# Performance work log

Measured on AMD Instinct MI355X. Metric: run time of the kernel, lower is better.

Reference implementation:

```python
import jax, jax.numpy as jnp
import numpy as np

N = 50000


def gcn_conv(x, ei, W, b, n_nodes):
    """PyG GCNConv with default add_self_loops=True, symmetric normalization."""
    h = x @ W  # [N, hidden]
    loop = jnp.arange(n_nodes, dtype=ei.dtype)
    src = jnp.concatenate([ei[0], loop])
    dst = jnp.concatenate([ei[1], loop])
    # degree over destination nodes, unit edge weights (incl. self loops)
    deg = jax.ops.segment_sum(jnp.ones(src.shape[0], dtype=h.dtype), dst, num_segments=n_nodes)
    dinv = jnp.where(deg > 0, jax.lax.rsqrt(deg), 0.0)
    norm = dinv[src] * dinv[dst]  # [E+N]
    out = jax.ops.segment_sum(norm[:, None] * h[src], dst, num_segments=n_nodes)
    return out + b


def setup_inputs() -> dict:
    key = jax.random.key(0)
    ks = jax.random.split(key, 16)
    d_in, hidden, d_out, E = 64, 64, 3, 800000
    inp = {
        "x": jax.random.normal(ks[0], (N, d_in), dtype=jnp.float32),
        "ei_spring": jax.random.randint(ks[1], (2, E), 0, N, dtype=jnp.int32),
        "ei_damper": jax.random.randint(ks[2], (2, E), 0, N, dtype=jnp.int32),
        "W1s": jax.random.normal(ks[3], (d_in, hidden), dtype=jnp.float32) / np.sqrt(d_in),
        "b1s": jnp.zeros((hidden,), dtype=jnp.float32),
        "W1d": jax.random.normal(ks[4], (d_in, hidden), dtype=jnp.float32) / np.sqrt(d_in),
        "b1d": jnp.zeros((hidden,), dtype=jnp.float32),
        "W2s": jax.random.normal(ks[5], (hidden, hidden), dtype=jnp.float32) / np.sqrt(hidden),
        "b2s": jnp.zeros((hidden,), dtype=jnp.float32),
        "W2d": jax.random.normal(ks[6], (hidden, hidden), dtype=jnp.float32) / np.sqrt(hidden),
        "b2d": jnp.zeros((hidden,), dtype=jnp.float32),
        "Wlin": jax.random.normal(ks[7], (hidden, d_out), dtype=jnp.float32) / np.sqrt(hidden),
        "blin": jnp.zeros((d_out,), dtype=jnp.float32),
    }
    return inp


def reference(x, ei_spring, ei_damper, W1s, b1s, W1d, b1d, W2s, b2s, W2d, b2d, Wlin, blin):
    # layer 1: HeteroConv sum over both relations, then ReLU
    h = gcn_conv(x, ei_spring, W1s, b1s, N) + gcn_conv(x, ei_damper, W1d, b1d, N)
    h = jax.nn.relu(h)
    # layer 2
    h = gcn_conv(h, ei_spring, W2s, b2s, N) + gcn_conv(h, ei_damper, W2d, b2d, N)
    h = jax.nn.relu(h)
    return h @ Wlin + blin
```

## Files before the change

### kernel.cpp

```cpp
#include <hip/hip_runtime.h>
#include <hip/hip_fp16.h>

#define NN 50000
#define BSHIFT 8
#define NBK ((NN + 255) >> 8)
#define CHUNK 4096
#define CAP 8192

typedef __attribute__((ext_vector_type(8))) _Float16 f16x8;
typedef __attribute__((ext_vector_type(4))) float f32x4;

__device__ __forceinline__ float recw(unsigned r) {
    unsigned short us = (unsigned short)(r >> 16);
    __half h;
    __builtin_memcpy(&h, &us, 2);
    return __half2float(h);
}
__device__ __forceinline__ float2 h2f2(unsigned v) {
    __half2 h;
    __builtin_memcpy(&h, &v, 4);
    return __half22float2(h);
}
__device__ __forceinline__ unsigned f2h2(float a, float b) {
    __half2 h = __floats2half2_rn(a, b);
    unsigned u;
    __builtin_memcpy(&u, &h, 4);
    return u;
}
__device__ __forceinline__ f16x8 as_f16x8(uint4 v) {
    f16x8 r;
    __builtin_memcpy(&r, &v, 16);
    return r;
}
__device__ __forceinline__ unsigned short f2h1(float v) {
    __half h = __float2half(v);
    unsigned short us;
    __builtin_memcpy(&us, &h, 2);
    return us;
}


__global__ __launch_bounds__(256) void cvt_x(const float* __restrict__ x,
                                             unsigned* __restrict__ x16, int total4) {
    int i = blockIdx.x * 256 + threadIdx.x;
    if (i >= total4) return;
    float4 v = reinterpret_cast<const float4*>(x)[i];
    uint2 o;
    o.x = f2h2(v.x, v.y);
    o.y = f2h2(v.z, v.w);
    reinterpret_cast<uint2*>(x16)[i] = o;
}


__global__ __launch_bounds__(256) void prep_w(const float* __restrict__ W1s,
                                              const float* __restrict__ W1d,
                                              const float* __restrict__ W2s,
                                              const float* __restrict__ W2d,
                                              unsigned short* __restrict__ Bp) {
    int idx = blockIdx.x * 256 + threadIdx.x;
    if (idx >= 16384) return;
    int layer = idx >> 13;
    int rem = idx & 8191;
    int j = rem & 7;
    int l = (rem >> 3) & 63;
    int jt = (rem >> 9) & 3;
    int ks = rem >> 11;
    int k = ks * 32 + (l >> 4) * 8 + j;
    int col = jt * 16 + (l & 15);
    const float* Ws = layer ? W2s : W1s;
    const float* Wd = layer ? W2d : W1d;
    float v = (k < 64) ? Ws[k * 64 + col] : Wd[(k - 64) * 64 + col];
    Bp[idx] = f2h1(v);
}


__global__ __launch_bounds__(256) void bucket_count(const int* __restrict__ eiS, int Es,
                                                    const int* __restrict__ eiD, int Ed,
                                                    int* __restrict__ cntS,
                                                    int* __restrict__ cntD) {
    __shared__ int h[NBK];
    int rel = blockIdx.y;
    const int* dst = rel ? (eiD + Ed) : (eiS + Es);
    int E = rel ? Ed : Es;
    int* cnt = rel ? cntD : cntS;
    int base = blockIdx.x * CHUNK;
    if (base >= E) return;
    for (int i = threadIdx.x; i < NBK; i += 256) h[i] = 0;
    __syncthreads();
    int end = (base + CHUNK < E) ? base + CHUNK : E;
    for (int e = base + threadIdx.x; e < end; e += 256)
        atomicAdd(&h[dst[e] >> BSHIFT], 1);
    __syncthreads();
    for (int i = threadIdx.x; i < NBK; i += 256)
        if (h[i]) atomicAdd(&cnt[i], h[i]);
}


__global__ __launch_bounds__(256) void bucket_scan(const int* __restrict__ cntS,
                                                   const int* __restrict__ cntD,
                                                   int* __restrict__ baseS,
                                                   int* __restrict__ baseD,
                                                   int* __restrict__ curS,
                                                   int* __restrict__ curD,
                                                   int* __restrict__ offsS,
                                                   int* __restrict__ offsD) {
    __shared__ int sA[256], sB[256];
    const int* cnt = blockIdx.x ? cntD : cntS;
    int* base = blockIdx.x ? baseD : baseS;
    int* cur  = blockIdx.x ? curD : curS;
    int* offs = blockIdx.x ? offsD : offsS;
    int t = threadIdx.x;
    int v = (t < NBK) ? cnt[t] : 0;
    sA[t] = v;
    __syncthreads();
    int* pin = sA; int* pout = sB;
    for (int st = 1; st < 256; st <<= 1) {
        int x = pin[t];
        if (t >= st) x += pin[t - st];
        pout[t] = x;
        __syncthreads();
        int* tmp = pin; pin = pout; pout = tmp;
    }
    int incl = pin[t];
    int excl = incl - v;
    if (t < NBK) { base[t] = excl; cur[t] = excl; }
    if (t == NBK - 1) { base[NBK] = incl; offs[NN] = incl; }
}


__global__ __launch_bounds__(256) void bucket_scatter(const int* __restrict__ eiS, int Es,
                                                      const int* __restrict__ eiD, int Ed,
                                                      int* __restrict__ curS,
                                                      int* __restrict__ curD,
                                                      unsigned* __restrict__ recS,
                                                      unsigned* __restrict__ recD) {
    __shared__ int h[NBK];
    __shared__ int rb[NBK];
    int rel = blockIdx.y;
    const int* ei = rel ? eiD : eiS;
    int E = rel ? Ed : Es;
    int* cur = rel ? curD : curS;
    unsigned* rec = rel ? recD : recS;
    int base = blockIdx.x * CHUNK;
    if (base >= E) return;
    const int* src = ei;
    const int* dst = ei + E;
    int end = (base + CHUNK < E) ? base + CHUNK : E;

    for (int i = threadIdx.x; i < NBK; i += 256) h[i] = 0;
    __syncthreads();
    for (int e = base + threadIdx.x; e < end; e += 256)
        atomicAdd(&h[dst[e] >> BSHIFT], 1);
    __syncthreads();
    for (int i = threadIdx.x; i < NBK; i += 256) {
        int c = h[i];
        rb[i] = c ? atomicAdd(&cur[i], c) : 0;
    }
    __syncthreads();
    for (int i = threadIdx.x; i < NBK; i += 256) h[i] = 0;
    __syncthreads();
    for (int e = base + threadIdx.x; e < end; e += 256) {
        int d = dst[e];
        int s = src[e];
        int b = d >> BSHIFT;
        int p = atomicAdd(&h[b], 1);
        rec[rb[b] + p] = (unsigned)s | ((unsigned)(d & 255) << 16);
    }
}


__global__ __launch_bounds__(256) void bucket_finalize(const int* __restrict__ baseS,
                                                       const int* __restrict__ baseD,
                                                       unsigned* __restrict__ recS,
                                                       unsigned* __restrict__ recD,
                                                       int* __restrict__ offsS,
                                                       int* __restrict__ offsD,
                                                       float* __restrict__ dinvS,
                                                       float* __restrict__ dinvD) {
    __shared__ unsigned recs[CAP];
    __shared__ int lc[256], sA[256], sB[256];
    int rel = blockIdx.y;
    const int* base = rel ? baseD : baseS;
    unsigned* rec = rel ? recD : recS;
    int* offs = rel ? offsD : offsS;
    float* dinv = rel ? dinvD : dinvS;
    int b = blockIdx.x;
    int b0 = base[b], b1 = base[b + 1];
    int cnt = b1 - b0;
    int t = threadIdx.x;
    lc[t] = 0;
    __syncthreads();
    for (int i = t; i < cnt; i += 256) {
        unsigned r = rec[b0 + i];
        if (i < CAP) recs[i] = r;
        atomicAdd(&lc[r >> 16], 1);
    }
    __syncthreads();
    int v = lc[t];
    int g = (b << BSHIFT) + t;
    if (g < NN) dinv[g] = rsqrtf((float)v + 1.0f);
    sA[t] = v;
    __syncthreads();
    int* pin = sA; int* pout = sB;
    for (int st = 1; st < 256; st <<= 1) {
        int x = pin[t];
        if (t >= st) x += pin[t - st];
        pout[t] = x;
        __syncthreads();
        int* tmp = pin; pin = pout; pout = tmp;
    }
    int excl = pin[t] - v;
    if (g < NN) offs[g] = b0 + excl;
    lc[t] = excl;
    __syncthreads();
    for (int i = t; i < cnt; i += 256) {
        unsigned r = (i < CAP) ? recs[i] : rec[b0 + i];
        int p = atomicAdd(&lc[r >> 16], 1);
        rec[b0 + p] = r & 0xFFFFu;
    }
}


__global__ __launch_bounds__(256) void pack_rec(unsigned* __restrict__ recS, int Es,
                                                unsigned* __restrict__ recD, int Ed,
                                                const float* __restrict__ dinvS,
                                                const float* __restrict__ dinvD) {
    int i = blockIdx.x * 256 + threadIdx.x;
    if (i < Es) {
        unsigned s = recS[i] & 0xFFFFu;
        recS[i] = s | ((unsigned)f2h1(dinvS[s]) << 16);
    }
    if (i < Ed) {
        unsigned s = recD[i] & 0xFFFFu;
        recD[i] = s | ((unsigned)f2h1(dinvD[s]) << 16);
    }
}


__global__ __launch_bounds__(256) void gather_agg(const int* __restrict__ offsS,
                                                  const unsigned* __restrict__ recS,
                                                  const int* __restrict__ offsD,
                                                  const unsigned* __restrict__ recD,
                                                  const unsigned* __restrict__ feat,
                                                  const float* __restrict__ dinvS,
                                                  const float* __restrict__ dinvD,
                                                  unsigned* __restrict__ A, int n) {
    int wid = (blockIdx.x * 256 + threadIdx.x) >> 6;
    int lane = threadIdx.x & 63;
    if (wid >= n) return;
    int g = lane >> 4;
    int q = lane & 15;

    const uint2* featv = reinterpret_cast<const uint2*>(feat);

    float dS = dinvS[wid];
    float dD = dinvD[wid];

    int eS0 = offsS[wid], eS1 = offsS[wid + 1];
    int eD0 = offsD[wid], eD1 = offsD[wid + 1];
    int nbS = (eS1 - eS0 + 3) >> 2;
    int nbD = (eD1 - eD0 + 3) >> 2;

    uint2 sv = featv[(size_t)wid * 16 + q];
    float2 s0 = h2f2(sv.x), s1 = h2f2(sv.y);
    float wself = (g == 0) ? dS : 0.0f;
    float wselfD = (g == 0) ? dD : 0.0f;
    float aS0 = wself * s0.x, aS1 = wself * s0.y, aS2 = wself * s1.x, aS3 = wself * s1.y;
    float aD0 = wselfD * s0.x, aD1 = wselfD * s0.y, aD2 = wselfD * s1.x, aD3 = wselfD * s1.y;

#define BODY_S(I)                                                              \
    {                                                                          \
        int e = eS0 + 4 * (I) + g;                                             \
        unsigned r = (e < eS1) ? recS[e] : 0u;                                 \
        uint2 v = featv[(size_t)(r & 0xFFFFu) * 16 + q];                       \
        float w = recw(r);                                                     \
        float2 f0 = h2f2(v.x), f1 = h2f2(v.y);                                 \
        aS0 = fmaf(w, f0.x, aS0); aS1 = fmaf(w, f0.y, aS1);                    \
        aS2 = fmaf(w, f1.x, aS2); aS3 = fmaf(w, f1.y, aS3);                    \
    }
#define BODY_D(I)                                                              \
    {                                                                          \
        int e = eD0 + 4 * (I) + g;                                             \
        unsigned r = (e < eD1) ? recD[e] : 0u;                                 \
        uint2 v = featv[(size_t)(r & 0xFFFFu) * 16 + q];                       \
        float w = recw(r);                                                     \
        float2 f0 = h2f2(v.x), f1 = h2f2(v.y);                                 \
        aD0 = fmaf(w, f0.x, aD0); aD1 = fmaf(w, f0.y, aD1);                    \
        aD2 = fmaf(w, f1.x, aD2); aD3 = fmaf(w, f1.y, aD3);                    \
    }

    int nb = (nbS < nbD) ? nbS : nbD;
    int i = 0;
#pragma unroll 2
    for (; i < nb; i++) {
        BODY_S(i)
        BODY_D(i)
    }
#pragma unroll 2
    for (int is = i; is < nbS; is++) BODY_S(is)
#pragma unroll 2
    for (int id = i; id < nbD; id++) BODY_D(id)

#undef BODY_S
#undef BODY_D

#pragma unroll
    for (int st = 16; st <= 32; st <<= 1) {
        aS0 += __shfl_xor(aS0, st, 64);
        aS1 += __shfl_xor(aS1, st, 64);
        aS2 += __shfl_xor(aS2, st, 64);
        aS3 += __shfl_xor(aS3, st, 64);
        aD0 += __shfl_xor(aD0, st, 64);
        aD1 += __shfl_xor(aD1, st, 64);
        aD2 += __shfl_xor(aD2, st, 64);
        aD3 += __shfl_xor(aD3, st, 64);
    }

    if (g == 0) {
        uint2 oS, oD;
        oS.x = f2h2(dS * aS0, dS * aS1);
        oS.y = f2h2(dS * aS2, dS * aS3);
        oD.x = f2h2(dD * aD0, dD * aD1);
        oD.y = f2h2(dD * aD2, dD * aD3);
        reinterpret_cast<uint2*>(A + (size_t)wid * 64)[q] = oS;
        reinterpret_cast<uint2*>(A + (size_t)wid * 64 + 32)[q] = oD;
    }
}


#define STORE_JT(ACC, JT)                                                     \
    {                                                                         \
        int colj = (JT) * 16 + lr;                                            \
        float bs = ba[colj] + bb[colj];                                       \
        _Pragma("unroll")                                                     \
        for (int r = 0; r < 4; r++) {                                         \
            float v = fmaxf(ACC[r] + bs, 0.0f);                               \
            outH[(size_t)(m0 + lh * 4 + r) * 64 + colj] = f2h1(v);            \
        }                                                                     \
    }

#define HEAD_JT(ACC, JT)                                                      \
    {                                                                         \
        int colj = (JT) * 16 + lr;                                            \
        float bs = ba[colj] + bb[colj];                                       \
        float w0 = Wlin[colj * 3 + 0];                                        \
        float w1 = Wlin[colj * 3 + 1];                                        \
        float w2 = Wlin[colj * 3 + 2];                                        \
        _Pragma("unroll")                                                     \
        for (int r = 0; r < 4; r++) {                                         \
            float v = fmaxf(ACC[r] + bs, 0.0f);                               \
            h0[r] = fmaf(v, w0, h0[r]);                                       \
            h1[r] = fmaf(v, w1, h1[r]);                                       \
            h2[r] = fmaf(v, w2, h2[r]);                                       \
        }                                                                     \
    }

template <int HEAD>
__global__ __launch_bounds__(256) void apply_mfma(const unsigned* __restrict__ A,
                                                  const unsigned short* __restrict__ Bp,
                                                  const float* __restrict__ ba,
                                                  const float* __restrict__ bb,
                                                  const float* __restrict__ Wlin,
                                                  const float* __restrict__ blin,
                                                  unsigned short* __restrict__ outH,
                                                  float* __restrict__ out3, int n) {
    int wid = (blockIdx.x * 256 + threadIdx.x) >> 6;
    int l = threadIdx.x & 63;
    int m0 = wid * 16;
    if (m0 >= n) return;
    int lr = l & 15;
    int lh = l >> 4;

    const uint4* Bv = reinterpret_cast<const uint4*>(Bp);
    f32x4 acc0 = {0.f, 0.f, 0.f, 0.f};
    f32x4 acc1 = {0.f, 0.f, 0.f, 0.f};
    f32x4 acc2 = {0.f, 0.f, 0.f, 0.f};
    f32x4 acc3 = {0.f, 0.f, 0.f, 0.f};

#pragma unroll
    for (int ks = 0; ks < 4; ks++) {
        uint4 av = *reinterpret_cast<const uint4*>(A + (size_t)(m0 + lr) * 64 + ks * 16 + lh * 4);
        f16x8 af = as_f16x8(av);
        uint4 b0 = Bv[(ks * 4 + 0) * 64 + l];
        uint4 b1 = Bv[(ks * 4 + 1) * 64 + l];
        uint4 b2 = Bv[(ks * 4 + 2) * 64 + l];
        uint4 b3 = Bv[(ks * 4 + 3) * 64 + l];
        acc0 = __builtin_amdgcn_mfma_f32_16x16x32_f16(af, as_f16x8(b0), acc0, 0, 0, 0);
        acc1 = __builtin_amdgcn_mfma_f32_16x16x32_f16(af, as_f16x8(b1), acc1, 0, 0, 0);
        acc2 = __builtin_amdgcn_mfma_f32_16x16x32_f16(af, as_f16x8(b2), acc2, 0, 0, 0);
        acc3 = __builtin_amdgcn_mfma_f32_16x16x32_f16(af, as_f16x8(b3), acc3, 0, 0, 0);
    }

    if (HEAD == 0) {
        STORE_JT(acc0, 0)
        STORE_JT(acc1, 1)
        STORE_JT(acc2, 2)
        STORE_JT(acc3, 3)
    } else {
        float h0[4] = {0.f, 0.f, 0.f, 0.f};
        float h1[4] = {0.f, 0.f, 0.f, 0.f};
        float h2[4] = {0.f, 0.f, 0.f, 0.f};
        HEAD_JT(acc0, 0)
        HEAD_JT(acc1, 1)
        HEAD_JT(acc2, 2)
        HEAD_JT(acc3, 3)
#pragma unroll
        for (int st = 1; st < 16; st <<= 1) {
#pragma unroll
            for (int r = 0; r < 4; r++) {
                h0[r] += __shfl_xor(h0[r], st, 64);
                h1[r] += __shfl_xor(h1[r], st, 64);
                h2[r] += __shfl_xor(h2[r], st, 64);
            }
        }
        if (lr == 0) {
#pragma unroll
            for (int r = 0; r < 4; r++) {
                int row = m0 + lh * 4 + r;
                out3[row * 3 + 0] = h0[r] + blin[0];
                out3[row * 3 + 1] = h1[r] + blin[1];
                out3[row * 3 + 2] = h2[r] + blin[2];
            }
        }
    }
}

extern "C" void kernel_launch(void* const* d_in, const int* in_sizes, int n_in,
                              void* d_out, int out_size, void* d_ws, size_t ws_size,
                              hipStream_t stream) {
    const float* x    = (const float*)d_in[0];
    const int*   eis  = (const int*)d_in[1];
    const int*   eid  = (const int*)d_in[2];
    const float* W1s  = (const float*)d_in[3];
    const float* b1s  = (const float*)d_in[4];
    const float* W1d  = (const float*)d_in[5];
    const float* b1d  = (const float*)d_in[6];
    const float* W2s  = (const float*)d_in[7];
    const float* b2s  = (const float*)d_in[8];
    const float* W2d  = (const float*)d_in[9];
    const float* b2d  = (const float*)d_in[10];
    const float* Wlin = (const float*)d_in[11];
    const float* blin = (const float*)d_in[12];

    const int N  = NN;
    const int Es = in_sizes[1] / 2;
    const int Ed = in_sizes[2] / 2;
    int Emax = (Es > Ed) ? Es : Ed;

    int*   cntS  = (int*)d_ws;
    int*   cntD  = cntS + NBK;
    int*   baseS = cntD + NBK;
    int*   baseD = baseS + (NBK + 4);
    int*   curS  = baseD + (NBK + 4);
    int*   curD  = curS + NBK;
    int*   offsS = curD + NBK;
    int*   offsD = offsS + (N + 4);
    float* dinvS = (float*)(offsD + (N + 4));
    float* dinvD = dinvS + N;
    unsigned* recS = (unsigned*)(dinvD + N);
    unsigned* recD = recS + Es;
    unsigned* x16  = recD + Ed;
    unsigned* h16u = x16 + (size_t)N * 32;
    unsigned* Abuf = h16u + (size_t)N * 32;
    unsigned short* Bp = (unsigned short*)(Abuf + (size_t)N * 64);
    unsigned short* h16 = (unsigned short*)h16u;

    hipMemsetAsync(cntS, 0, (size_t)2 * NBK * sizeof(int), stream);
    cvt_x<<<(N * 16 + 255) / 256, 256, 0, stream>>>(x, x16, N * 16);
    prep_w<<<64, 256, 0, stream>>>(W1s, W1d, W2s, W2d, Bp);
    dim3 egrid((Emax + CHUNK - 1) / CHUNK, 2);
    bucket_count<<<egrid, 256, 0, stream>>>(eis, Es, eid, Ed, cntS, cntD);
    bucket_scan<<<2, 256, 0, stream>>>(cntS, cntD, baseS, baseD, curS, curD, offsS, offsD);
    bucket_scatter<<<egrid, 256, 0, stream>>>(eis, Es, eid, Ed, curS, curD, recS, recD);
    dim3 fgrid(NBK, 2);
    bucket_finalize<<<fgrid, 256, 0, stream>>>(baseS, baseD, recS, recD, offsS, offsD,
                                               dinvS, dinvD);
    pack_rec<<<(Emax + 255) / 256, 256, 0, stream>>>(recS, Es, recD, Ed, dinvS, dinvD);

    int gatherBlocks = (N * 64 + 255) / 256;
    int mtiles = (N + 15) / 16;
    int applyBlocks = (mtiles * 64 + 255) / 256;

    gather_agg<<<gatherBlocks, 256, 0, stream>>>(offsS, recS, offsD, recD, x16,
                                                 dinvS, dinvD, Abuf, N);
    apply_mfma<0><<<applyBlocks, 256, 0, stream>>>(Abuf, Bp, b1s, b1d,
                                                   nullptr, nullptr, h16, nullptr, N);

    gather_agg<<<gatherBlocks, 256, 0, stream>>>(offsS, recS, offsD, recD, h16u,
                                                 dinvS, dinvD, Abuf, N);
    apply_mfma<1><<<applyBlocks, 256, 0, stream>>>(Abuf, Bp + 8192, b2s, b2d,
                                                   Wlin, blin, nullptr, (float*)d_out, N);
}
```

Measured before the change: 176.9 us.

## Merge prep kernels and remap gather to one node per quarter-wave per relation

Fuses x conversion, weight packing and bucket counting into one launch with a 3-row grid, removing two kernel launches. Gather now assigns each 16-lane group its own node and relation, using a 2D grid over relations, so there is no cross-group shuffle reduction. Each group loops over its own edge list in steps of four, with a wave-wide any() to handle divergent degrees. This removes the shuffles and spreads work over more waves, at the cost of divergence across the four nodes in a wave and a larger prep grid where many blocks exit early.

```diff
diff --git a/kernel.cpp b/kernel.cpp
--- a/kernel.cpp
+++ b/kernel.cpp
@@ -40,59 +40,58 @@
 }
 
 
-__global__ __launch_bounds__(256) void cvt_x(const float* __restrict__ x,
-                                             unsigned* __restrict__ x16, int total4) {
-    int i = blockIdx.x * 256 + threadIdx.x;
-    if (i >= total4) return;
-    float4 v = reinterpret_cast<const float4*>(x)[i];
-    uint2 o;
-    o.x = f2h2(v.x, v.y);
-    o.y = f2h2(v.z, v.w);
-    reinterpret_cast<uint2*>(x16)[i] = o;
-}
-
-
-__global__ __launch_bounds__(256) void prep_w(const float* __restrict__ W1s,
-                                              const float* __restrict__ W1d,
-                                              const float* __restrict__ W2s,
-                                              const float* __restrict__ W2d,
-                                              unsigned short* __restrict__ Bp) {
-    int idx = blockIdx.x * 256 + threadIdx.x;
-    if (idx >= 16384) return;
-    int layer = idx >> 13;
-    int rem = idx & 8191;
-    int j = rem & 7;
-    int l = (rem >> 3) & 63;
-    int jt = (rem >> 9) & 3;
-    int ks = rem >> 11;
-    int k = ks * 32 + (l >> 4) * 8 + j;
-    int col = jt * 16 + (l & 15);
-    const float* Ws = layer ? W2s : W1s;
-    const float* Wd = layer ? W2d : W1d;
-    float v = (k < 64) ? Ws[k * 64 + col] : Wd[(k - 64) * 64 + col];
-    Bp[idx] = f2h1(v);
-}
-
-
-__global__ __launch_bounds__(256) void bucket_count(const int* __restrict__ eiS, int Es,
-                                                    const int* __restrict__ eiD, int Ed,
-                                                    int* __restrict__ cntS,
-                                                    int* __restrict__ cntD) {
+__global__ __launch_bounds__(256) void fat_prep(const int* __restrict__ eiS, int Es,
+                                                const int* __restrict__ eiD, int Ed,
+                                                int* __restrict__ cntS,
+                                                int* __restrict__ cntD,
+                                                const float* __restrict__ x,
+                                                unsigned* __restrict__ x16, int total4,
+                                                const float* __restrict__ W1s,
+                                                const float* __restrict__ W1d,
+                                                const float* __restrict__ W2s,
+                                                const float* __restrict__ W2d,
+                                                unsigned short* __restrict__ Bp) {
     __shared__ int h[NBK];
-    int rel = blockIdx.y;
-    const int* dst = rel ? (eiD + Ed) : (eiS + Es);
-    int E = rel ? Ed : Es;
-    int* cnt = rel ? cntD : cntS;
-    int base = blockIdx.x * CHUNK;
-    if (base >= E) return;
-    for (int i = threadIdx.x; i < NBK; i += 256) h[i] = 0;
-    __syncthreads();
-    int end = (base + CHUNK < E) ? base + CHUNK : E;
-    for (int e = base + threadIdx.x; e < end; e += 256)
-        atomicAdd(&h[dst[e] >> BSHIFT], 1);
-    __syncthreads();
-    for (int i = threadIdx.x; i < NBK; i += 256)
-        if (h[i]) atomicAdd(&cnt[i], h[i]);
+    if (blockIdx.y < 2) {
+        int rel = blockIdx.y;
+        const int* dst = rel ? (eiD + Ed) : (eiS + Es);
+        int E = rel ? Ed : Es;
+        int* cnt = rel ? cntD : cntS;
+        int base = blockIdx.x * CHUNK;
+        if (base >= E) return;
+        for (int i = threadIdx.x; i < NBK; i += 256) h[i] = 0;
+        __syncthreads();
+        int end = (base + CHUNK < E) ? base + CHUNK : E;
+        for (int e = base + threadIdx.x; e < end; e += 256)
+            atomicAdd(&h[dst[e] >> BSHIFT], 1);
+        __syncthreads();
+        for (int i = threadIdx.x; i < NBK; i += 256)
+            if (h[i]) atomicAdd(&cnt[i], h[i]);
+    } else {
+        int i = blockIdx.x * 256 + threadIdx.x;
+        if (i < total4) {
+            float4 v = reinterpret_cast<const float4*>(x)[i];
+            uint2 o;
+            o.x = f2h2(v.x, v.y);
+            o.y = f2h2(v.z, v.w);
+            reinterpret_cast<uint2*>(x16)[i] = o;
+        }
+        if (blockIdx.x < 64) {
+            int idx = blockIdx.x * 256 + threadIdx.x;
+            int layer = idx >> 13;
+            int rem = idx & 8191;
+            int j = rem & 7;
+            int l = (rem >> 3) & 63;
+            int jt = (rem >> 9) & 3;
+            int ks = rem >> 11;
+            int k = ks * 32 + (l >> 4) * 8 + j;
+            int col = jt * 16 + (l & 15);
+            const float* Ws = layer ? W2s : W1s;
+            const float* Wd = layer ? W2d : W1d;
+            float v = (k < 64) ? Ws[k * 64 + col] : Wd[(k - 64) * 64 + col];
+            Bp[idx] = f2h1(v);
+        }
+    }
 }
 
 
@@ -245,86 +244,49 @@
                                                   const float* __restrict__ dinvS,
                                                   const float* __restrict__ dinvD,
                                                   unsigned* __restrict__ A, int n) {
-    int wid = (blockIdx.x * 256 + threadIdx.x) >> 6;
+    int rel = blockIdx.y;
+    const int* __restrict__ offs = rel ? offsD : offsS;
+    const unsigned* __restrict__ rec = rel ? recD : recS;
+    const float* __restrict__ dinv = rel ? dinvD : dinvS;
+
+    int wv = (blockIdx.x * 256 + threadIdx.x) >> 6;
     int lane = threadIdx.x & 63;
-    if (wid >= n) return;
-    int g = lane >> 4;
+    int c = lane >> 4;
     int q = lane & 15;
+    int node = wv * 4 + c;
+    if (node >= n) return;
 
     const uint2* featv = reinterpret_cast<const uint2*>(feat);
 
-    float dS = dinvS[wid];
-    float dD = dinvD[wid];
-
-    int eS0 = offsS[wid], eS1 = offsS[wid + 1];
-    int eD0 = offsD[wid], eD1 = offsD[wid + 1];
-    int nbS = (eS1 - eS0 + 3) >> 2;
-    int nbD = (eD1 - eD0 + 3) >> 2;
-
-    uint2 sv = featv[(size_t)wid * 16 + q];
+    float dv = dinv[node];
+    int e0 = offs[node];
+    int cnt = offs[node + 1] - e0;
+
+    uint2 sv = featv[(size_t)node * 16 + q];
     float2 s0 = h2f2(sv.x), s1 = h2f2(sv.y);
-    float wself = (g == 0) ? dS : 0.0f;
-    float wselfD = (g == 0) ? dD : 0.0f;
-    float aS0 = wself * s0.x, aS1 = wself * s0.y, aS2 = wself * s1.x, aS3 = wself * s1.y;
-    float aD0 = wselfD * s0.x, aD1 = wselfD * s0.y, aD2 = wselfD * s1.x, aD3 = wselfD * s1.y;
-
-#define BODY_S(I)                                                              \
-    {                                                                          \
-        int e = eS0 + 4 * (I) + g;                                             \
-        unsigned r = (e < eS1) ? recS[e] : 0u;                                 \
-        uint2 v = featv[(size_t)(r & 0xFFFFu) * 16 + q];                       \
-        float w = recw(r);                                                     \
-        float2 f0 = h2f2(v.x), f1 = h2f2(v.y);                                 \
-        aS0 = fmaf(w, f0.x, aS0); aS1 = fmaf(w, f0.y, aS1);                    \
-        aS2 = fmaf(w, f1.x, aS2); aS3 = fmaf(w, f1.y, aS3);                    \
-    }
-#define BODY_D(I)                                                              \
-    {                                                                          \
-        int e = eD0 + 4 * (I) + g;                                             \
-        unsigned r = (e < eD1) ? recD[e] : 0u;                                 \
-        uint2 v = featv[(size_t)(r & 0xFFFFu) * 16 + q];                       \
-        float w = recw(r);                                                     \
-        float2 f0 = h2f2(v.x), f1 = h2f2(v.y);                                 \
-        aD0 = fmaf(w, f0.x, aD0); aD1 = fmaf(w, f0.y, aD1);                    \
-        aD2 = fmaf(w, f1.x, aD2); aD3 = fmaf(w, f1.y, aD3);                    \
-    }
-
-    int nb = (nbS < nbD) ? nbS : nbD;
+    float a0 = dv * s0.x, a1 = dv * s0.y, a2 = dv * s1.x, a3 = dv * s1.y;
+
     int i = 0;
-#pragma unroll 2
-    for (; i < nb; i++) {
-        BODY_S(i)
-        BODY_D(i)
-    }
-#pragma unroll 2
-    for (int is = i; is < nbS; is++) BODY_S(is)
-#pragma unroll 2
-    for (int id = i; id < nbD; id++) BODY_D(id)
-
-#undef BODY_S
-#undef BODY_D
-
+    while (__any(i < cnt)) {
 #pragma unroll
-    for (int st = 16; st <= 32; st <<= 1) {
-        aS0 += __shfl_xor(aS0, st, 64);
-        aS1 += __shfl_xor(aS1, st, 64);
-        aS2 += __shfl_xor(aS2, st, 64);
-        aS3 += __shfl_xor(aS3, st, 64);
-        aD0 += __shfl_xor(aD0, st, 64);
-        aD1 += __shfl_xor(aD1, st, 64);
-        aD2 += __shfl_xor(aD2, st, 64);
-        aD3 += __shfl_xor(aD3, st, 64);
-    }
-
-    if (g == 0) {
-        uint2 oS, oD;
-        oS.x = f2h2(dS * aS0, dS * aS1);
-        oS.y = f2h2(dS * aS2, dS * aS3);
-        oD.x = f2h2(dD * aD0, dD * aD1);
-        oD.y = f2h2(dD * aD2, dD * aD3);
-        reinterpret_cast<uint2*>(A + (size_t)wid * 64)[q] = oS;
-        reinterpret_cast<uint2*>(A + (size_t)wid * 64 + 32)[q] = oD;
-    }
+        for (int k = 0; k < 4; k++) {
+            int e = i + k;
+            unsigned r = (e < cnt) ? rec[e0 + e] : 0u;
+            uint2 v = featv[(size_t)(r & 0xFFFFu) * 16 + q];
+            float wt = recw(r);
+            float2 f0 = h2f2(v.x), f1 = h2f2(v.y);
+            a0 = fmaf(wt, f0.x, a0);
+            a1 = fmaf(wt, f0.y, a1);
+            a2 = fmaf(wt, f1.x, a2);
+            a3 = fmaf(wt, f1.y, a3);
+        }
+        i += 4;
+    }
+
+    uint2 o;
+    o.x = f2h2(dv * a0, dv * a1);
+    o.y = f2h2(dv * a2, dv * a3);
+    reinterpret_cast<uint2*>(A)[(size_t)node * 32 + rel * 16 + q] = o;
 }
 
 
@@ -466,28 +428,28 @@
     unsigned short* h16 = (unsigned short*)h16u;
 
     hipMemsetAsync(cntS, 0, (size_t)2 * NBK * sizeof(int), stream);
-    cvt_x<<<(N * 16 + 255) / 256, 256, 0, stream>>>(x, x16, N * 16);
-    prep_w<<<64, 256, 0, stream>>>(W1s, W1d, W2s, W2d, Bp);
+    dim3 pgrid(3125, 3);
+    fat_prep<<<pgrid, 256, 0, stream>>>(eis, Es, eid, Ed, cntS, cntD,
+                                        x, x16, N * 16, W1s, W1d, W2s, W2d, Bp);
+    bucket_scan<<<2, 256, 0, stream>>>(cntS, cntD, baseS, baseD, curS, curD, offsS, offsD);
     dim3 egrid((Emax + CHUNK - 1) / CHUNK, 2);
-    bucket_count<<<egrid, 256, 0, stream>>>(eis, Es, eid, Ed, cntS, cntD);
-    bucket_scan<<<2, 256, 0, stream>>>(cntS, cntD, baseS, baseD, curS, curD, offsS, offsD);
     bucket_scatter<<<egrid, 256, 0, stream>>>(eis, Es, eid, Ed, curS, curD, recS, recD);
     dim3 fgrid(NBK, 2);
     bucket_finalize<<<fgrid, 256, 0, stream>>>(baseS, baseD, recS, recD, offsS, offsD,
                                                dinvS, dinvD);
     pack_rec<<<(Emax + 255) / 256, 256, 0, stream>>>(recS, Es, recD, Ed, dinvS, dinvD);
 
-    int gatherBlocks = (N * 64 + 255) / 256;
+    dim3 ggrid((N + 15) / 16, 2);
     int mtiles = (N + 15) / 16;
     int applyBlocks = (mtiles * 64 + 255) / 256;
 
-    gather_agg<<<gatherBlocks, 256, 0, stream>>>(offsS, recS, offsD, recD, x16,
-                                                 dinvS, dinvD, Abuf, N);
+    gather_agg<<<ggrid, 256, 0, stream>>>(offsS, recS, offsD, recD, x16,
+                                          dinvS, dinvD, Abuf, N);
     apply_mfma<0><<<applyBlocks, 256, 0, stream>>>(Abuf, Bp, b1s, b1d,
                                                    nullptr, nullptr, h16, nullptr, N);
 
-    gather_agg<<<gatherBlocks, 256, 0, stream>>>(offsS, recS, offsD, recD, h16u,
-                                                 dinvS, dinvD, Abuf, N);
+    gather_agg<<<ggrid, 256, 0, stream>>>(offsS, recS, offsD, recD, h16u,
+                                          dinvS, dinvD, Abuf, N);
     apply_mfma<1><<<applyBlocks, 256, 0, stream>>>(Abuf, Bp + 8192, b2s, b2d,
                                                    Wlin, blin, nullptr, (float*)d_out, N);
 }
```

Result: no change. 178.6 us (+1.0%).

## Fuse prep kernels, compute degrees early, fold dinv packing into finalize

Applied to the files above, without the earlier changes.

Merges x conversion, weight packing and bucket counting into one launch, and adds global atomic degree counting there so dinv can be computed in the scan kernel. The finalize kernel then writes the fp16 dinv of each source directly into the sorted records, which removes the separate pack_rec pass over all edges. This cuts three launches and one full read-write pass of the edge records. In exchange it adds global atomics on degree counters and a larger memset. Many grid blocks in the count part exit immediately, since the grid is sized for the x conversion.

```diff
diff --git a/kernel.cpp b/kernel.cpp
--- a/kernel.cpp
+++ b/kernel.cpp
@@ -40,59 +40,64 @@
 }
 
 
-__global__ __launch_bounds__(256) void cvt_x(const float* __restrict__ x,
-                                             unsigned* __restrict__ x16, int total4) {
-    int i = blockIdx.x * 256 + threadIdx.x;
-    if (i >= total4) return;
-    float4 v = reinterpret_cast<const float4*>(x)[i];
-    uint2 o;
-    o.x = f2h2(v.x, v.y);
-    o.y = f2h2(v.z, v.w);
-    reinterpret_cast<uint2*>(x16)[i] = o;
-}
-
-
-__global__ __launch_bounds__(256) void prep_w(const float* __restrict__ W1s,
-                                              const float* __restrict__ W1d,
-                                              const float* __restrict__ W2s,
-                                              const float* __restrict__ W2d,
-                                              unsigned short* __restrict__ Bp) {
-    int idx = blockIdx.x * 256 + threadIdx.x;
-    if (idx >= 16384) return;
-    int layer = idx >> 13;
-    int rem = idx & 8191;
-    int j = rem & 7;
-    int l = (rem >> 3) & 63;
-    int jt = (rem >> 9) & 3;
-    int ks = rem >> 11;
-    int k = ks * 32 + (l >> 4) * 8 + j;
-    int col = jt * 16 + (l & 15);
-    const float* Ws = layer ? W2s : W1s;
-    const float* Wd = layer ? W2d : W1d;
-    float v = (k < 64) ? Ws[k * 64 + col] : Wd[(k - 64) * 64 + col];
-    Bp[idx] = f2h1(v);
-}
-
-
-__global__ __launch_bounds__(256) void bucket_count(const int* __restrict__ eiS, int Es,
-                                                    const int* __restrict__ eiD, int Ed,
-                                                    int* __restrict__ cntS,
-                                                    int* __restrict__ cntD) {
+__global__ __launch_bounds__(256) void fat_prep(const int* __restrict__ eiS, int Es,
+                                                const int* __restrict__ eiD, int Ed,
+                                                int* __restrict__ cntS,
+                                                int* __restrict__ cntD,
+                                                int* __restrict__ degS,
+                                                int* __restrict__ degD,
+                                                const float* __restrict__ x,
+                                                unsigned* __restrict__ x16, int total4,
+                                                const float* __restrict__ W1s,
+                                                const float* __restrict__ W1d,
+                                                const float* __restrict__ W2s,
+                                                const float* __restrict__ W2d,
+                                                unsigned short* __restrict__ Bp) {
     __shared__ int h[NBK];
-    int rel = blockIdx.y;
-    const int* dst = rel ? (eiD + Ed) : (eiS + Es);
-    int E = rel ? Ed : Es;
-    int* cnt = rel ? cntD : cntS;
-    int base = blockIdx.x * CHUNK;
-    if (base >= E) return;
-    for (int i = threadIdx.x; i < NBK; i += 256) h[i] = 0;
-    __syncthreads();
-    int end = (base + CHUNK < E) ? base + CHUNK : E;
-    for (int e = base + threadIdx.x; e < end; e += 256)
-        atomicAdd(&h[dst[e] >> BSHIFT], 1);
-    __syncthreads();
-    for (int i = threadIdx.x; i < NBK; i += 256)
-        if (h[i]) atomicAdd(&cnt[i], h[i]);
+    if (blockIdx.y < 2) {
+        int rel = blockIdx.y;
+        const int* dst = rel ? (eiD + Ed) : (eiS + Es);
+        int E = rel ? Ed : Es;
+        int* cnt = rel ? cntD : cntS;
+        int* deg = rel ? degD : degS;
+        int base = blockIdx.x * CHUNK;
+        if (base >= E) return;
+        for (int i = threadIdx.x; i < NBK; i += 256) h[i] = 0;
+        __syncthreads();
+        int end = (base + CHUNK < E) ? base + CHUNK : E;
+        for (int e = base + threadIdx.x; e < end; e += 256) {
+            int d = dst[e];
+            atomicAdd(&h[d >> BSHIFT], 1);
+            atomicAdd(&deg[d], 1);
+        }
+        __syncthreads();
+        for (int i = threadIdx.x; i < NBK; i += 256)
+            if (h[i]) atomicAdd(&cnt[i], h[i]);
+    } else {
+        int i = blockIdx.x * 256 + threadIdx.x;
+        if (i < total4) {
+            float4 v = reinterpret_cast<const float4*>(x)[i];
+            uint2 o;
+            o.x = f2h2(v.x, v.y);
+            o.y = f2h2(v.z, v.w);
+            reinterpret_cast<uint2*>(x16)[i] = o;
+        }
+        if (blockIdx.x < 64) {
+            int idx = blockIdx.x * 256 + threadIdx.x;
+            int layer = idx >> 13;
+            int rem = idx & 8191;
+            int j = rem & 7;
+            int l = (rem >> 3) & 63;
+            int jt = (rem >> 9) & 3;
+            int ks = rem >> 11;
+            int k = ks * 32 + (l >> 4) * 8 + j;
+            int col = jt * 16 + (l & 15);
+            const float* Ws = layer ? W2s : W1s;
+            const float* Wd = layer ? W2d : W1d;
+            float v = (k < 64) ? Ws[k * 64 + col] : Wd[(k - 64) * 64 + col];
+            Bp[idx] = f2h1(v);
+        }
+    }
 }
 
 
@@ -103,13 +108,26 @@
                                                    int* __restrict__ curS,
                                                    int* __restrict__ curD,
                                                    int* __restrict__ offsS,
-                                                   int* __restrict__ offsD) {
+                                                   int* __restrict__ offsD,
+                                                   const int* __restrict__ degS,
+                                                   const int* __restrict__ degD,
+                                                   float* __restrict__ dinvS,
+                                                   float* __restrict__ dinvD) {
+    int t = threadIdx.x;
+    if (blockIdx.x >= 2) {
+        int g = (blockIdx.x - 2) * 256 + t;
+        if (g < NN) {
+            dinvS[g] = rsqrtf((float)degS[g] + 1.0f);
+            dinvD[g] = rsqrtf((float)degD[g] + 1.0f);
+        }
+        return;
+    }
     __shared__ int sA[256], sB[256];
-    const int* cnt = blockIdx.x ? cntD : cntS;
-    int* base = blockIdx.x ? baseD : baseS;
-    int* cur  = blockIdx.x ? curD : curS;
-    int* offs = blockIdx.x ? offsD : offsS;
-    int t = threadIdx.x;
+    int r = blockIdx.x;
+    const int* cnt = r ? cntD : cntS;
+    int* base = r ? baseD : baseS;
+    int* cur  = r ? curD : curS;
+    int* offs = r ? offsD : offsS;
     int v = (t < NBK) ? cnt[t] : 0;
     sA[t] = v;
     __syncthreads();
@@ -175,15 +193,15 @@
                                                        unsigned* __restrict__ recD,
                                                        int* __restrict__ offsS,
                                                        int* __restrict__ offsD,
-                                                       float* __restrict__ dinvS,
-                                                       float* __restrict__ dinvD) {
+                                                       const float* __restrict__ dinvS,
+                                                       const float* __restrict__ dinvD) {
     __shared__ unsigned recs[CAP];
     __shared__ int lc[256], sA[256], sB[256];
     int rel = blockIdx.y;
     const int* base = rel ? baseD : baseS;
     unsigned* rec = rel ? recD : recS;
     int* offs = rel ? offsD : offsS;
-    float* dinv = rel ? dinvD : dinvS;
+    const float* dinv = rel ? dinvD : dinvS;
     int b = blockIdx.x;
     int b0 = base[b], b1 = base[b + 1];
     int cnt = b1 - b0;
@@ -198,7 +216,6 @@
     __syncthreads();
     int v = lc[t];
     int g = (b << BSHIFT) + t;
-    if (g < NN) dinv[g] = rsqrtf((float)v + 1.0f);
     sA[t] = v;
     __syncthreads();
     int* pin = sA; int* pout = sB;
@@ -216,23 +233,8 @@
     for (int i = t; i < cnt; i += 256) {
         unsigned r = (i < CAP) ? recs[i] : rec[b0 + i];
         int p = atomicAdd(&lc[r >> 16], 1);
-        rec[b0 + p] = r & 0xFFFFu;
-    }
-}
-
-
-__global__ __launch_bounds__(256) void pack_rec(unsigned* __restrict__ recS, int Es,
-                                                unsigned* __restrict__ recD, int Ed,
-                                                const float* __restrict__ dinvS,
-                                                const float* __restrict__ dinvD) {
-    int i = blockIdx.x * 256 + threadIdx.x;
-    if (i < Es) {
-        unsigned s = recS[i] & 0xFFFFu;
-        recS[i] = s | ((unsigned)f2h1(dinvS[s]) << 16);
-    }
-    if (i < Ed) {
-        unsigned s = recD[i] & 0xFFFFu;
-        recD[i] = s | ((unsigned)f2h1(dinvD[s]) << 16);
+        unsigned s = r & 0xFFFFu;
+        rec[b0 + p] = s | ((unsigned)f2h1(dinv[s]) << 16);
     }
 }
 
@@ -449,7 +451,9 @@
 
     int*   cntS  = (int*)d_ws;
     int*   cntD  = cntS + NBK;
-    int*   baseS = cntD + NBK;
+    int*   degS  = cntD + NBK;
+    int*   degD  = degS + N;
+    int*   baseS = degD + N;
     int*   baseD = baseS + (NBK + 4);
     int*   curS  = baseD + (NBK + 4);
     int*   curD  = curS + NBK;
@@ -465,17 +469,17 @@
     unsigned short* Bp = (unsigned short*)(Abuf + (size_t)N * 64);
     unsigned short* h16 = (unsigned short*)h16u;
 
-    hipMemsetAsync(cntS, 0, (size_t)2 * NBK * sizeof(int), stream);
-    cvt_x<<<(N * 16 + 255) / 256, 256, 0, stream>>>(x, x16, N * 16);
-    prep_w<<<64, 256, 0, stream>>>(W1s, W1d, W2s, W2d, Bp);
+    hipMemsetAsync(cntS, 0, ((size_t)2 * NBK + (size_t)2 * N) * sizeof(int), stream);
+    dim3 pgrid(3125, 3);
+    fat_prep<<<pgrid, 256, 0, stream>>>(eis, Es, eid, Ed, cntS, cntD, degS, degD,
+                                        x, x16, N * 16, W1s, W1d, W2s, W2d, Bp);
+    bucket_scan<<<2 + NBK, 256, 0, stream>>>(cntS, cntD, baseS, baseD, curS, curD,
+                                             offsS, offsD, degS, degD, dinvS, dinvD);
     dim3 egrid((Emax + CHUNK - 1) / CHUNK, 2);
-    bucket_count<<<egrid, 256, 0, stream>>>(eis, Es, eid, Ed, cntS, cntD);
-    bucket_scan<<<2, 256, 0, stream>>>(cntS, cntD, baseS, baseD, curS, curD, offsS, offsD);
     bucket_scatter<<<egrid, 256, 0, stream>>>(eis, Es, eid, Ed, curS, curD, recS, recD);
     dim3 fgrid(NBK, 2);
     bucket_finalize<<<fgrid, 256, 0, stream>>>(baseS, baseD, recS, recD, offsS, offsD,
                                                dinvS, dinvD);
-    pack_rec<<<(Emax + 255) / 256, 256, 0, stream>>>(recS, Es, recD, Ed, dinvS, dinvD);
 
     int gatherBlocks = (N * 64 + 255) / 256;
     int mtiles = (N + 15) / 16;
```

Result: slower. 222.3 us (+25.7%).

## Sub-bucket edges by source range and fuse prep kernels into one launch

Applied to the files above, without the earlier changes.

The edge bucketing now classifies each edge by destination bucket and also by source range (8 sub-classes), so records within a destination bucket are grouped by source. The aim is better locality on the source-feature gathers in the aggregation. The count, x conversion and weight packing kernels are merged into one multi-role launch to cut launch overhead. The scan now runs serially over about 1600 classes in chunks, and the shared histograms are 8x larger, which adds LDS pressure and atomic work. The finalize kernel may re-sort within each bucket, which would undo part of the source grouping.

```diff
diff --git a/kernel.cpp b/kernel.cpp
--- a/kernel.cpp
+++ b/kernel.cpp
@@ -4,6 +4,9 @@
 #define NN 50000
 #define BSHIFT 8
 #define NBK ((NN + 255) >> 8)
+#define NR 8
+#define RSH 13
+#define NCLS (NBK * NR)
 #define CHUNK 4096
 #define CAP 8192
 
@@ -40,91 +43,111 @@
 }
 
 
-__global__ __launch_bounds__(256) void cvt_x(const float* __restrict__ x,
-                                             unsigned* __restrict__ x16, int total4) {
-    int i = blockIdx.x * 256 + threadIdx.x;
-    if (i >= total4) return;
-    float4 v = reinterpret_cast<const float4*>(x)[i];
-    uint2 o;
-    o.x = f2h2(v.x, v.y);
-    o.y = f2h2(v.z, v.w);
-    reinterpret_cast<uint2*>(x16)[i] = o;
-}
-
-
-__global__ __launch_bounds__(256) void prep_w(const float* __restrict__ W1s,
-                                              const float* __restrict__ W1d,
-                                              const float* __restrict__ W2s,
-                                              const float* __restrict__ W2d,
-                                              unsigned short* __restrict__ Bp) {
-    int idx = blockIdx.x * 256 + threadIdx.x;
-    if (idx >= 16384) return;
-    int layer = idx >> 13;
-    int rem = idx & 8191;
-    int j = rem & 7;
-    int l = (rem >> 3) & 63;
-    int jt = (rem >> 9) & 3;
-    int ks = rem >> 11;
-    int k = ks * 32 + (l >> 4) * 8 + j;
-    int col = jt * 16 + (l & 15);
-    const float* Ws = layer ? W2s : W1s;
-    const float* Wd = layer ? W2d : W1d;
-    float v = (k < 64) ? Ws[k * 64 + col] : Wd[(k - 64) * 64 + col];
-    Bp[idx] = f2h1(v);
-}
-
-
-__global__ __launch_bounds__(256) void bucket_count(const int* __restrict__ eiS, int Es,
-                                                    const int* __restrict__ eiD, int Ed,
-                                                    int* __restrict__ cntS,
-                                                    int* __restrict__ cntD) {
-    __shared__ int h[NBK];
-    int rel = blockIdx.y;
-    const int* dst = rel ? (eiD + Ed) : (eiS + Es);
-    int E = rel ? Ed : Es;
-    int* cnt = rel ? cntD : cntS;
-    int base = blockIdx.x * CHUNK;
-    if (base >= E) return;
-    for (int i = threadIdx.x; i < NBK; i += 256) h[i] = 0;
-    __syncthreads();
-    int end = (base + CHUNK < E) ? base + CHUNK : E;
-    for (int e = base + threadIdx.x; e < end; e += 256)
-        atomicAdd(&h[dst[e] >> BSHIFT], 1);
-    __syncthreads();
-    for (int i = threadIdx.x; i < NBK; i += 256)
-        if (h[i]) atomicAdd(&cnt[i], h[i]);
-}
-
-
-__global__ __launch_bounds__(256) void bucket_scan(const int* __restrict__ cntS,
-                                                   const int* __restrict__ cntD,
-                                                   int* __restrict__ baseS,
-                                                   int* __restrict__ baseD,
-                                                   int* __restrict__ curS,
-                                                   int* __restrict__ curD,
-                                                   int* __restrict__ offsS,
-                                                   int* __restrict__ offsD) {
-    __shared__ int sA[256], sB[256];
+__global__ __launch_bounds__(256) void fat_prep(const int* __restrict__ eiS, int Es,
+                                                const int* __restrict__ eiD, int Ed,
+                                                int* __restrict__ cntS,
+                                                int* __restrict__ cntD,
+                                                const float* __restrict__ x,
+                                                unsigned* __restrict__ x16, int total4,
+                                                const float* __restrict__ W1s,
+                                                const float* __restrict__ W1d,
+                                                const float* __restrict__ W2s,
+                                                const float* __restrict__ W2d,
+                                                unsigned short* __restrict__ Bp) {
+    __shared__ int h[NCLS];
+    if (blockIdx.y < 2) {
+        int rel = blockIdx.y;
+        const int* ei = rel ? eiD : eiS;
+        int E = rel ? Ed : Es;
+        int* cnt = rel ? cntD : cntS;
+        int base = blockIdx.x * CHUNK;
+        if (base >= E) return;
+        const int* src = ei;
+        const int* dst = ei + E;
+        for (int i = threadIdx.x; i < NCLS; i += 256) h[i] = 0;
+        __syncthreads();
+        int end = (base + CHUNK < E) ? base + CHUNK : E;
+        for (int e = base + threadIdx.x; e < end; e += 256) {
+            int cls = (dst[e] >> BSHIFT) * NR + (src[e] >> RSH);
+            atomicAdd(&h[cls], 1);
+        }
+        __syncthreads();
+        for (int i = threadIdx.x; i < NCLS; i += 256)
+            if (h[i]) atomicAdd(&cnt[i], h[i]);
+    } else {
+        int i = blockIdx.x * 256 + threadIdx.x;
+        if (i < total4) {
+            float4 v = reinterpret_cast<const float4*>(x)[i];
+            uint2 o;
+            o.x = f2h2(v.x, v.y);
+            o.y = f2h2(v.z, v.w);
+            reinterpret_cast<uint2*>(x16)[i] = o;
+        }
+        if (blockIdx.x < 64) {
+            int idx = blockIdx.x * 256 + threadIdx.x;
+            int layer = idx >> 13;
+            int rem = idx & 8191;
+            int j = rem & 7;
+            int l = (rem >> 3) & 63;
+            int jt = (rem >> 9) & 3;
+            int ks = rem >> 11;
+            int k = ks * 32 + (l >> 4) * 8 + j;
+            int col = jt * 16 + (l & 15);
+            const float* Ws = layer ? W2s : W1s;
+            const float* Wd = layer ? W2d : W1d;
+            float v = (k < 64) ? Ws[k * 64 + col] : Wd[(k - 64) * 64 + col];
+            Bp[idx] = f2h1(v);
+        }
+    }
+}
+
+
+__global__ __launch_bounds__(256) void cls_scan(const int* __restrict__ cntS,
+                                                const int* __restrict__ cntD,
+                                                int* __restrict__ baseS,
+                                                int* __restrict__ baseD,
+                                                int* __restrict__ curS,
+                                                int* __restrict__ curD,
+                                                int* __restrict__ offsS,
+                                                int* __restrict__ offsD) {
     const int* cnt = blockIdx.x ? cntD : cntS;
     int* base = blockIdx.x ? baseD : baseS;
     int* cur  = blockIdx.x ? curD : curS;
     int* offs = blockIdx.x ? offsD : offsS;
+    __shared__ int sA[256], sB[256];
+    __shared__ int carry_s;
     int t = threadIdx.x;
-    int v = (t < NBK) ? cnt[t] : 0;
-    sA[t] = v;
-    __syncthreads();
-    int* pin = sA; int* pout = sB;
-    for (int st = 1; st < 256; st <<= 1) {
-        int x = pin[t];
-        if (t >= st) x += pin[t - st];
-        pout[t] = x;
+    if (t == 0) carry_s = 0;
+    __syncthreads();
+    int nchunk = (NCLS + 255) / 256;
+    for (int c = 0; c < nchunk; ++c) {
+        int i = c * 256 + t;
+        int v = (i < NCLS) ? cnt[i] : 0;
+        sA[t] = v;
         __syncthreads();
-        int* tmp = pin; pin = pout; pout = tmp;
-    }
-    int incl = pin[t];
-    int excl = incl - v;
-    if (t < NBK) { base[t] = excl; cur[t] = excl; }
-    if (t == NBK - 1) { base[NBK] = incl; offs[NN] = incl; }
+        int* pin = sA; int* pout = sB;
+        for (int st = 1; st < 256; st <<= 1) {
+            int x = pin[t];
+            if (t >= st) x += pin[t - st];
+            pout[t] = x;
+            __syncthreads();
+            int* tmp = pin; pin = pout; pout = tmp;
+        }
+        int incl = pin[t];
+        int b = carry_s;
+        if (i < NCLS) {
+            int excl = b + incl - v;
+            base[i] = excl;
+            cur[i] = excl;
+        }
+        __syncthreads();
+        if (t == 255) carry_s = b + incl;
+        __syncthreads();
+    }
+    if (t == 0) {
+        base[NCLS] = carry_s;
+        offs[NN] = carry_s;
+    }
 }
 
 
@@ -134,8 +157,8 @@
                                                       int* __restrict__ curD,
                                                       unsigned* __restrict__ recS,
                                                       unsigned* __restrict__ recD) {
-    __shared__ int h[NBK];
-    __shared__ int rb[NBK];
+    __shared__ int h[NCLS];
+    __shared__ int rb[NCLS];
     int rel = blockIdx.y;
     const int* ei = rel ? eiD : eiS;
     int E = rel ? Ed : Es;
@@ -147,24 +170,26 @@
     const int* dst = ei + E;
     int end = (base + CHUNK < E) ? base + CHUNK : E;
 
-    for (int i = threadIdx.x; i < NBK; i += 256) h[i] = 0;
-    __syncthreads();
-    for (int e = base + threadIdx.x; e < end; e += 256)
-        atomicAdd(&h[dst[e] >> BSHIFT], 1);
-    __syncthreads();
-    for (int i = threadIdx.x; i < NBK; i += 256) {
+    for (int i = threadIdx.x; i < NCLS; i += 256) h[i] = 0;
+    __syncthreads();
+    for (int e = base + threadIdx.x; e < end; e += 256) {
+        int cls = (dst[e] >> BSHIFT) * NR + (src[e] >> RSH);
+        atomicAdd(&h[cls], 1);
+    }
+    __syncthreads();
+    for (int i = threadIdx.x; i < NCLS; i += 256) {
         int c = h[i];
         rb[i] = c ? atomicAdd(&cur[i], c) : 0;
     }
     __syncthreads();
-    for (int i = threadIdx.x; i < NBK; i += 256) h[i] = 0;
+    for (int i = threadIdx.x; i < NCLS; i += 256) h[i] = 0;
     __syncthreads();
     for (int e = base + threadIdx.x; e < end; e += 256) {
         int d = dst[e];
         int s = src[e];
-        int b = d >> BSHIFT;
-        int p = atomicAdd(&h[b], 1);
-        rec[rb[b] + p] = (unsigned)s | ((unsigned)(d & 255) << 16);
+        int cls = (d >> BSHIFT) * NR + (s >> RSH);
+        int p = atomicAdd(&h[cls], 1);
+        rec[rb[cls] + p] = (unsigned)s | ((unsigned)(d & 255) << 16);
     }
 }
 
@@ -185,7 +210,7 @@
     int* offs = rel ? offsD : offsS;
     float* dinv = rel ? dinvD : dinvS;
     int b = blockIdx.x;
-    int b0 = base[b], b1 = base[b + 1];
+    int b0 = base[b * NR], b1 = base[(b + 1) * NR];
     int cnt = b1 - b0;
     int t = threadIdx.x;
     lc[t] = 0;
@@ -448,12 +473,12 @@
     int Emax = (Es > Ed) ? Es : Ed;
 
     int*   cntS  = (int*)d_ws;
-    int*   cntD  = cntS + NBK;
-    int*   baseS = cntD + NBK;
-    int*   baseD = baseS + (NBK + 4);
-    int*   curS  = baseD + (NBK + 4);
-    int*   curD  = curS + NBK;
-    int*   offsS = curD + NBK;
+    int*   cntD  = cntS + NCLS;
+    int*   baseS = cntD + NCLS;
+    int*   baseD = baseS + (NCLS + 4);
+    int*   curS  = baseD + (NCLS + 4);
+    int*   curD  = curS + NCLS;
+    int*   offsS = curD + NCLS;
     int*   offsD = offsS + (N + 4);
     float* dinvS = (float*)(offsD + (N + 4));
     float* dinvD = dinvS + N;
@@ -465,12 +490,12 @@
     unsigned short* Bp = (unsigned short*)(Abuf + (size_t)N * 64);
     unsigned short* h16 = (unsigned short*)h16u;
 
-    hipMemsetAsync(cntS, 0, (size_t)2 * NBK * sizeof(int), stream);
-    cvt_x<<<(N * 16 + 255) / 256, 256, 0, stream>>>(x, x16, N * 16);
-    prep_w<<<64, 256, 0, stream>>>(W1s, W1d, W2s, W2d, Bp);
+    hipMemsetAsync(cntS, 0, (size_t)2 * NCLS * sizeof(int), stream);
+    dim3 pgrid(3125, 3);
+    fat_prep<<<pgrid, 256, 0, stream>>>(eis, Es, eid, Ed, cntS, cntD,
+                                        x, x16, N * 16, W1s, W1d, W2s, W2d, Bp);
+    cls_scan<<<2, 256, 0, stream>>>(cntS, cntD, baseS, baseD, curS, curD, offsS, offsD);
     dim3 egrid((Emax + CHUNK - 1) / CHUNK, 2);
-    bucket_count<<<egrid, 256, 0, stream>>>(eis, Es, eid, Ed, cntS, cntD);
-    bucket_scan<<<2, 256, 0, stream>>>(cntS, cntD, baseS, baseD, curS, curD, offsS, offsD);
     bucket_scatter<<<egrid, 256, 0, stream>>>(eis, Es, eid, Ed, curS, curD, recS, recD);
     dim3 fgrid(NBK, 2);
     bucket_finalize<<<fgrid, 256, 0, stream>>>(baseS, baseD, recS, recD, offsS, offsD,
```

Measured after the change: 186.6 us. +5.5%, slower.
